# Performance work log

Hardware: AMD Instinct MI355X
Metric: run time of the kernel (lower is better)

The kernel has to match this reference:

```python
import jax, jax.numpy as jnp
import numpy as np

K = 3  # spatial kernel size (TVConv_k_square == 9)


def setup_inputs() -> dict:
    key = jax.random.key(0)
    k1, k2 = jax.random.split(key)
    B, C, H, W = 8, 96, 128, 128
    x = jax.random.normal(k1, (B, C, H, W), dtype=jnp.float32)
    weight_maps = jax.random.normal(k2, (1, C, K, K, H, W), dtype=jnp.float32)
    return {"x": x, "weight_maps": weight_maps}


def reference(x, weight_maps):
    # Per-pixel spatially-varying 3x3 depthwise conv.
    B, C, H, W = x.shape
    xp = jnp.pad(x, ((0, 0), (0, 0), (1, 1), (1, 1)))  # zero pad, (B,C,H+2,W+2)
    # Gather the 9 shifted views (equivalent to the as_strided unfold, stride 1).
    patches = jnp.stack(
        [xp[:, :, i:i + H, j:j + W] for i in range(K) for j in range(K)], axis=2
    ).reshape(B, C, K, K, H, W)
    # Weighted sum over the 3x3 window per channel per pixel.
    out = (weight_maps * patches).sum(axis=(2, 3))  # (B,C,H,W)
    return out
```

## Files before the change

### kernel.cpp

```cpp
#include <hip/hip_runtime.h>


namespace {
constexpr int B = 8, C = 96, H = 128, W = 128;
constexpr int HW = H * W;
}

typedef float f4 __attribute__((ext_vector_type(4)));

__global__ __launch_bounds__(256, 3) void tvconv_kernel(
    const float* __restrict__ x,
    const float* __restrict__ wm,
    float* __restrict__ out) {
  const int t  = threadIdx.x;
  const int c  = blockIdx.x >> 3;
  const int h0 = (blockIdx.x & 7) * 16;
  const int tr = t >> 5;
  const int w4 = t & 31;
  const int w  = w4 * 4;
  const int h  = h0 + tr * 2;
  const bool lower = ((tr & 1) == 0);

  const int hP = lower ? h : h + 1;
  const int hQ = lower ? h + 1 : h;

  f4 wtP[9], wtQ[9];
  {
    const float* wc = wm + (size_t)c * 9 * HW + w;
#pragma unroll
    for (int k = 0; k < 9; ++k) {
      const int ti = k / 3, tj = k % 3;
      const int kk = lower ? k : (6 - 3 * ti + tj);
      wtP[k] = __builtin_nontemporal_load(
          reinterpret_cast<const f4*>(wc + (size_t)kk * HW + hP * W));
      wtQ[k] = __builtin_nontemporal_load(
          reinterpret_cast<const f4*>(wc + (size_t)kk * HW + hQ * W));
    }
  }
  if (hP == 0 || hP == H - 1) { wtP[0] = 0.f; wtP[1] = 0.f; wtP[2] = 0.f; }

  const int offF = lower ? ((h == 0) ? 0 : -W)
                         : ((h == H - 2) ? W : 2 * W);
  const int offM = lower ? 0 : W;
  const int offN = lower ? W : 0;

  const bool at_left  = (w4 == 0);
  const bool at_right = (w4 == 31);

  const float* xb = x + (size_t)c * HW + h * W + w;
  float* obP = out + (size_t)c * HW + hP * W + w;
  float* obQ = out + (size_t)c * HW + hQ * W + w;

  f4 nF = *reinterpret_cast<const f4*>(xb + offF);
  f4 nM = *reinterpret_cast<const f4*>(xb + offM);
  f4 nN = *reinterpret_cast<const f4*>(xb + offN);

  auto make_xv = [&](float* xv, const f4 r) {
    float left  = __shfl_up(r.w, 1);
    float right = __shfl_down(r.x, 1);
    if (at_left)  left  = 0.f;
    if (at_right) right = 0.f;
    xv[0] = left; xv[1] = r.x; xv[2] = r.y; xv[3] = r.z; xv[4] = r.w;
    xv[5] = right;
  };
  auto acc_row = [&](float* acc, const f4* wt, const int i, const float* xv) {
#pragma unroll
    for (int j = 0; j < 3; ++j) {
      const f4 wv = wt[i * 3 + j];
      const float wa[4] = {wv.x, wv.y, wv.z, wv.w};
#pragma unroll
      for (int m = 0; m < 4; ++m) acc[m] += wa[m] * xv[m + j];
    }
  };

#pragma unroll
  for (int b = 0; b < B; ++b) {
    const f4 Lf = nF, Lm = nM, Ln = nN;
    if (b + 1 < B) {
      xb += (size_t)C * HW;
      nF = *reinterpret_cast<const f4*>(xb + offF);
      nM = *reinterpret_cast<const f4*>(xb + offM);
      nN = *reinterpret_cast<const f4*>(xb + offN);
    }

    f4 P;
    P.x = __shfl_xor(Ln.x, 32);
    P.y = __shfl_xor(Ln.y, 32);
    P.z = __shfl_xor(Ln.z, 32);
    P.w = __shfl_xor(Ln.w, 32);

    float xvF[6], xvM[6], xvN[6], xvP[6];
    make_xv(xvF, Lf);
    make_xv(xvM, Lm);
    make_xv(xvN, Ln);
    make_xv(xvP, P);

    float accP[4] = {0.f, 0.f, 0.f, 0.f};
    float accQ[4] = {0.f, 0.f, 0.f, 0.f};
    acc_row(accP, wtP, 0, xvF);
    acc_row(accP, wtP, 1, xvM);
    acc_row(accP, wtP, 2, xvN);
    acc_row(accQ, wtQ, 0, xvM);
    acc_row(accQ, wtQ, 1, xvN);
    acc_row(accQ, wtQ, 2, xvP);

    f4 oP, oQ;
    oP.x = accP[0]; oP.y = accP[1]; oP.z = accP[2]; oP.w = accP[3];
    oQ.x = accQ[0]; oQ.y = accQ[1]; oQ.z = accQ[2]; oQ.w = accQ[3];
    __builtin_nontemporal_store(oP, reinterpret_cast<f4*>(obP));
    __builtin_nontemporal_store(oQ, reinterpret_cast<f4*>(obQ));
    obP += (size_t)C * HW;
    obQ += (size_t)C * HW;
  }
}

extern "C" void kernel_launch(void* const* d_in, const int* in_sizes, int n_in,
                              void* d_out, int out_size, void* d_ws, size_t ws_size,
                              hipStream_t stream) {
  const float* x  = (const float*)d_in[0];
  const float* wm = (const float*)d_in[1];
  float* out = (float*)d_out;

  const int blocks = C * (H / 16);
  tvconv_kernel<<<blocks, 256, 0, stream>>>(x, wm, out);
}
```

Baseline: 138.2 us.

## Stage x rows in double-buffered LDS tile to share halo rows across waves

Each thread now loads only its own two rows of x per batch, plus edge waves loading one halo row, and writes them into a double-buffered shared-memory tile. Neighbouring up/down rows are read from LDS instead of being reloaded from global memory or exchanged via cross-lane shuffles. This removes redundant global reads of x but adds a block-wide barrier per batch iteration and LDS traffic.

```diff
diff --git a/kernel.cpp b/kernel.cpp
--- a/kernel.cpp
+++ b/kernel.cpp
@@ -4,6 +4,8 @@
 namespace {
 constexpr int B = 8, C = 96, H = 128, W = 128;
 constexpr int HW = H * W;
+constexpr int ROWS = 16;
+constexpr int SLOTS = 18;
 }
 
 typedef float f4 __attribute__((ext_vector_type(4)));
@@ -12,48 +14,42 @@
     const float* __restrict__ x,
     const float* __restrict__ wm,
     float* __restrict__ out) {
+  __shared__ __align__(16) float xs[2][SLOTS][W];
+
   const int t  = threadIdx.x;
   const int c  = blockIdx.x >> 3;
-  const int h0 = (blockIdx.x & 7) * 16;
+  const int h0 = (blockIdx.x & 7) * ROWS;
   const int tr = t >> 5;
   const int w4 = t & 31;
   const int w  = w4 * 4;
-  const int h  = h0 + tr * 2;
-  const bool lower = ((tr & 1) == 0);
+  const int r0 = h0 + 2 * tr;
+  const int r1 = r0 + 1;
 
-  const int hP = lower ? h : h + 1;
-  const int hQ = lower ? h + 1 : h;
+  const float* wc = wm + (size_t)c * 9 * HW + w;
+  f4 wtP[9], wtQ[9];
+#pragma unroll
+  for (int k = 0; k < 9; ++k) {
+    wtP[k] = __builtin_nontemporal_load(
+        reinterpret_cast<const f4*>(wc + (size_t)k * HW + r0 * W));
+    wtQ[k] = __builtin_nontemporal_load(
+        reinterpret_cast<const f4*>(wc + (size_t)k * HW + r1 * W));
+  }
+  if (r0 == 0)     { wtP[0] = 0.f; wtP[1] = 0.f; wtP[2] = 0.f; }
+  if (r1 == H - 1) { wtQ[6] = 0.f; wtQ[7] = 0.f; wtQ[8] = 0.f; }
 
-  f4 wtP[9], wtQ[9];
-  {
-    const float* wc = wm + (size_t)c * 9 * HW + w;
-#pragma unroll
-    for (int k = 0; k < 9; ++k) {
-      const int ti = k / 3, tj = k % 3;
-      const int kk = lower ? k : (6 - 3 * ti + tj);
-      wtP[k] = __builtin_nontemporal_load(
-          reinterpret_cast<const f4*>(wc + (size_t)kk * HW + hP * W));
-      wtQ[k] = __builtin_nontemporal_load(
-          reinterpret_cast<const f4*>(wc + (size_t)kk * HW + hQ * W));
-    }
-  }
-  if (hP == 0 || hP == H - 1) { wtP[0] = 0.f; wtP[1] = 0.f; wtP[2] = 0.f; }
-
-  const int offF = lower ? ((h == 0) ? 0 : -W)
-                         : ((h == H - 2) ? W : 2 * W);
-  const int offM = lower ? 0 : W;
-  const int offN = lower ? W : 0;
+  const bool up_halo  = (tr == 0);
+  const bool dn_halo  = (tr == 7);
+  const bool has_halo = up_halo || dn_halo;
+  const int halo_row  = up_halo ? max(h0 - 1, 0) : min(h0 + ROWS, H - 1);
+  const int halo_slot = up_halo ? 0 : (SLOTS - 1);
 
   const bool at_left  = (w4 == 0);
   const bool at_right = (w4 == 31);
 
-  const float* xb = x + (size_t)c * HW + h * W + w;
-  float* obP = out + (size_t)c * HW + hP * W + w;
-  float* obQ = out + (size_t)c * HW + hQ * W + w;
-
-  f4 nF = *reinterpret_cast<const f4*>(xb + offF);
-  f4 nM = *reinterpret_cast<const f4*>(xb + offM);
-  f4 nN = *reinterpret_cast<const f4*>(xb + offN);
+  const size_t bstride = (size_t)C * HW;
+  const float* xb = x + (size_t)c * HW + w;
+  float* ob0 = out + (size_t)c * HW + (size_t)r0 * W + w;
+  float* ob1 = ob0 + W;
 
   auto make_xv = [&](float* xv, const f4 r) {
     float left  = __shfl_up(r.w, 1);
@@ -73,44 +69,66 @@
     }
   };
 
+  f4 c0 = *reinterpret_cast<const f4*>(xb + (size_t)r0 * W);
+  f4 c1 = *reinterpret_cast<const f4*>(xb + (size_t)r1 * W);
+  f4 ch;
+  if (has_halo) ch = *reinterpret_cast<const f4*>(xb + (size_t)halo_row * W);
+  {
+    float* s = &xs[0][0][0];
+    *reinterpret_cast<f4*>(s + (2 * tr + 1) * W + w) = c0;
+    *reinterpret_cast<f4*>(s + (2 * tr + 2) * W + w) = c1;
+    if (has_halo) *reinterpret_cast<f4*>(s + halo_slot * W + w) = ch;
+  }
+  __syncthreads();
+
+  f4 n0, n1, nh;
 #pragma unroll
   for (int b = 0; b < B; ++b) {
-    const f4 Lf = nF, Lm = nM, Ln = nN;
     if (b + 1 < B) {
-      xb += (size_t)C * HW;
-      nF = *reinterpret_cast<const f4*>(xb + offF);
-      nM = *reinterpret_cast<const f4*>(xb + offM);
-      nN = *reinterpret_cast<const f4*>(xb + offN);
+      const float* xn = xb + bstride;
+      n0 = *reinterpret_cast<const f4*>(xn + (size_t)r0 * W);
+      n1 = *reinterpret_cast<const f4*>(xn + (size_t)r1 * W);
+      if (has_halo)
+        nh = *reinterpret_cast<const f4*>(xn + (size_t)halo_row * W);
+      xb = xn;
     }
 
-    f4 P;
-    P.x = __shfl_xor(Ln.x, 32);
-    P.y = __shfl_xor(Ln.y, 32);
-    P.z = __shfl_xor(Ln.z, 32);
-    P.w = __shfl_xor(Ln.w, 32);
+    const float* s = &xs[b & 1][0][0];
+    const f4 up = *reinterpret_cast<const f4*>(s + (2 * tr + 0) * W + w);
+    const f4 dn = *reinterpret_cast<const f4*>(s + (2 * tr + 3) * W + w);
 
-    float xvF[6], xvM[6], xvN[6], xvP[6];
-    make_xv(xvF, Lf);
-    make_xv(xvM, Lm);
-    make_xv(xvN, Ln);
-    make_xv(xvP, P);
+    float xvU[6], xv0[6], xv1[6], xvD[6];
+    make_xv(xvU, up);
+    make_xv(xv0, c0);
+    make_xv(xv1, c1);
+    make_xv(xvD, dn);
 
     float accP[4] = {0.f, 0.f, 0.f, 0.f};
     float accQ[4] = {0.f, 0.f, 0.f, 0.f};
-    acc_row(accP, wtP, 0, xvF);
-    acc_row(accP, wtP, 1, xvM);
-    acc_row(accP, wtP, 2, xvN);
-    acc_row(accQ, wtQ, 0, xvM);
-    acc_row(accQ, wtQ, 1, xvN);
-    acc_row(accQ, wtQ, 2, xvP);
+    acc_row(accP, wtP, 0, xvU);
+    acc_row(accP, wtP, 1, xv0);
+    acc_row(accP, wtP, 2, xv1);
+    acc_row(accQ, wtQ, 0, xv0);
+    acc_row(accQ, wtQ, 1, xv1);
+    acc_row(accQ, wtQ, 2, xvD);
 
     f4 oP, oQ;
     oP.x = accP[0]; oP.y = accP[1]; oP.z = accP[2]; oP.w = accP[3];
     oQ.x = accQ[0]; oQ.y = accQ[1]; oQ.z = accQ[2]; oQ.w = accQ[3];
-    __builtin_nontemporal_store(oP, reinterpret_cast<f4*>(obP));
-    __builtin_nontemporal_store(oQ, reinterpret_cast<f4*>(obQ));
-    obP += (size_t)C * HW;
-    obQ += (size_t)C * HW;
+    __builtin_nontemporal_store(oP, reinterpret_cast<f4*>(ob0));
+    __builtin_nontemporal_store(oQ, reinterpret_cast<f4*>(ob1));
+    ob0 += bstride;
+    ob1 += bstride;
+
+    if (b + 1 < B) {
+      float* d = &xs[(b + 1) & 1][0][0];
+      *reinterpret_cast<f4*>(d + (2 * tr + 1) * W + w) = n0;
+      *reinterpret_cast<f4*>(d + (2 * tr + 2) * W + w) = n1;
+      if (has_halo) *reinterpret_cast<f4*>(d + halo_slot * W + w) = nh;
+      __syncthreads();
+      c0 = n0;
+      c1 = n1;
+    }
   }
 }
 
@@ -121,6 +139,6 @@
   const float* wm = (const float*)d_in[1];
   float* out = (float*)d_out;
 
-  const int blocks = C * (H / 16);
+  const int blocks = C * (H / ROWS);
   tvconv_kernel<<<blocks, 256, 0, stream>>>(x, wm, out);
 }
```

Result: no change. 138.0 us (-0.1%).
